# Kernel optimization log

Measured on AMD Instinct MI355X. Metric: run time of the kernel, lower is better.

The kernel has to match this reference:

```python
import jax, jax.numpy as jnp
import numpy as np

B, T, D, H = 4, 1024, 1024, 16


def setup_inputs() -> dict:
    key = jax.random.key(0)
    ks = jax.random.split(key, 6)
    s = 0.02  # small init so softmax is well-conditioned
    return {
        "x": jax.random.normal(ks[0], (B, T, D), jnp.float32),
        "position_embedding": jax.random.normal(ks[1], (B, T, D), jnp.float32),
        "Wc": jax.random.normal(ks[2], (2 * D, D), jnp.float32) * s,
        "bc": jnp.zeros((2 * D,), jnp.float32),
        "Wp": jax.random.normal(ks[3], (D, D), jnp.float32) * s,
        "bp": jnp.zeros((D,), jnp.float32),
        "Wo": jax.random.normal(ks[4], (D, D), jnp.float32) * s,
        "bo": jnp.zeros((D,), jnp.float32),
        "num_heads": H,
    }


def reference(x, position_embedding, Wc, bc, Wp, bp, Wo, bo, num_heads):
    b, t, d = x.shape
    h = num_heads
    hd = d // h
    scale = hd ** -0.5
    # content projection -> q, k  (value reuses content k, as in the original)
    cqk = (x @ Wc.T + bc).reshape(b, t, 2, h, hd)
    q = cqk[:, :, 0]  # [B,T,H,hd]
    k = cqk[:, :, 1]  # [B,T,H,hd]
    # position keys
    pk = (position_embedding @ Wp.T + bp).reshape(b, t, h, hd)
    # dual-stream scores: content-content + content-position
    scores = (jnp.einsum('bqhd,bkhd->bhqk', q, k)
              + jnp.einsum('bqhd,bkhd->bhqk', q, pk)) * scale
    attn = jax.nn.softmax(scores, axis=-1)  # dropout is identity in eval
    out = jnp.einsum('bhqk,bkhd->bqhd', attn, k).reshape(b, t, d)
    return out @ Wo.T + bo, attn
```

## Files before the change

### kernel.cpp

```cpp
#include <hip/hip_runtime.h>
#include <hip/hip_bf16.h>

#define BB 4
#define TT 1024
#define DD 1024
#define HH 16
#define HDIM 64
#define MM (BB*TT)

typedef unsigned short u16;
typedef __attribute__((ext_vector_type(8))) short bf16x8;
typedef __attribute__((ext_vector_type(8))) _Float16 f16x8;
typedef __attribute__((ext_vector_type(4))) float f32x4;
typedef __attribute__((ext_vector_type(4))) unsigned short u16x4;

__device__ __forceinline__ u16 f2bf(float f) {
    union { float f; unsigned u; } v; v.f = f;
    return (u16)((v.u + 0x7fffu + ((v.u >> 16) & 1u)) >> 16);
}
__device__ __forceinline__ float bf2f(u16 h) {
    union { unsigned u; float f; } v; v.u = ((unsigned)h) << 16; return v.f;
}
__device__ __forceinline__ u16 f2h(float f) {
    union { _Float16 h; u16 u; } v; v.h = (_Float16)f;
    return v.u;
}

__device__ __forceinline__ void gload16(const void* g, void* l) {
    __builtin_amdgcn_global_load_lds(
        (const __attribute__((address_space(1))) unsigned int*)g,
        (__attribute__((address_space(3))) unsigned int*)l, 16, 0, 0);
}

__device__ __forceinline__ void cvt_body(const float* __restrict__ src,
                                         u16* __restrict__ dst,
                                         int bid, bool to_fp16)
{
    const size_t i = ((size_t)bid * 256 + threadIdx.x) * 4;
    const float4 v = *(const float4*)&src[i];
    u16x4 o;
    if (to_fp16) { o[0] = f2h(v.x); o[1] = f2h(v.y); o[2] = f2h(v.z); o[3] = f2h(v.w); }
    else         { o[0] = f2bf(v.x); o[1] = f2bf(v.y); o[2] = f2bf(v.z); o[3] = f2bf(v.w); }
    *(u16x4*)&dst[i] = o;
}

__global__ __launch_bounds__(256)
void cvt1_kernel(const float* __restrict__ x, u16* __restrict__ x16,
                 const float* __restrict__ Wc, u16* __restrict__ Wc16)
{
    const int bid = blockIdx.x;
    if (bid < 4096) cvt_body(x, x16, bid, true);
    else            cvt_body(Wc, Wc16, bid - 4096, true);
}

__global__ __launch_bounds__(256)
void cvt2_kernel(const float* __restrict__ pe, u16* __restrict__ pe16,
                 const float* __restrict__ Wp, u16* __restrict__ Wp16,
                 const float* __restrict__ Wo, u16* __restrict__ Wo16)
{
    const int bid = blockIdx.x;
    if (bid < 4096)      cvt_body(pe, pe16, bid, true);
    else if (bid < 5120) cvt_body(Wp, Wp16, bid - 4096, true);
    else                 cvt_body(Wo, Wo16, bid - 5120, false);
}

__global__ __launch_bounds__(256)
void ktrans_kernel(const u16* __restrict__ k16, u16* __restrict__ k16T)
{
    __shared__ u16 tmp[64][72];
    const int tc = blockIdx.x, h = blockIdx.y, b = blockIdx.z;
    const size_t hb = ((size_t)(b * HH + h)) << 16;
    const int tid = threadIdx.x;
    const int sr = tid >> 2, sc = (tid & 3) * 8;
    *(bf16x8*)&tmp[sr][sc]      = *(const bf16x8*)&k16[hb + (size_t)(tc * 64 + sr) * HDIM + sc];
    *(bf16x8*)&tmp[sr][sc + 32] = *(const bf16x8*)&k16[hb + (size_t)(tc * 64 + sr) * HDIM + sc + 32];
    __syncthreads();
#pragma unroll
    for (int half = 0; half < 2; ++half) {
        bf16x8 v;
#pragma unroll
        for (int j = 0; j < 8; ++j) v[j] = (short)tmp[sc + half * 32 + j][sr];
        *(bf16x8*)&k16T[hb + (size_t)sr * TT + tc * 64 + sc + half * 32] = v;
    }
}

template<bool FP16, int MODE>
__global__ __launch_bounds__(256)
void gemm_mfma(const u16* __restrict__ Ah, const u16* __restrict__ Bh,
               const float* __restrict__ bias,
               float* __restrict__ dstF, u16* __restrict__ dstH1,
               const u16* __restrict__ kaux16,
               const int M, const int N, const int K)
{
    __shared__ u16 As[128][64];
    __shared__ u16 Bs[128][64];

    const int tid  = threadIdx.x;
    const int w    = tid >> 6;
    const int lane = tid & 63;
    const int lg   = lane >> 4;
    const int lr   = lane & 15;
    const int wr   = w >> 1, wc = w & 1;
    const int m0   = blockIdx.y * 128, n0 = blockIdx.x * 128;

    const f32x4 zero = {0.f, 0.f, 0.f, 0.f};
    f32x4 acc[4][4];
#pragma unroll
    for (int i = 0; i < 4; ++i)
#pragma unroll
        for (int j = 0; j < 4; ++j) acc[i][j] = zero;

    const int srow = tid >> 3;
    const int scol = (tid & 7) * 8;
    const int ldr  = w << 3;

    for (int k0 = 0; k0 < K; k0 += 64) {
        __syncthreads();
#pragma unroll
        for (int i = 0; i < 4; ++i) {
            const size_t ga = (size_t)(m0 + i * 32 + srow) * K + k0 + scol;
            const size_t gb = (size_t)(n0 + i * 32 + srow) * K + k0 + scol;
            gload16(&Ah[ga], &As[i * 32 + ldr][0]);
            gload16(&Bh[gb], &Bs[i * 32 + ldr][0]);
        }
        __syncthreads();
#pragma unroll
        for (int kk = 0; kk < 2; ++kk) {
            const int koff = kk * 32 + lg * 8;
#pragma unroll
            for (int mf = 0; mf < 4; ++mf) {
#pragma unroll
                for (int nf = 0; nf < 4; ++nf) {
                    if constexpr (FP16) {
                        const f16x8 a = *(const f16x8*)&As[wr * 64 + mf * 16 + lr][koff];
                        const f16x8 b = *(const f16x8*)&Bs[wc * 64 + nf * 16 + lr][koff];
                        acc[mf][nf] = __builtin_amdgcn_mfma_f32_16x16x32_f16(a, b, acc[mf][nf], 0, 0, 0);
                    } else {
                        const bf16x8 a = *(const bf16x8*)&As[wr * 64 + mf * 16 + lr][koff];
                        const bf16x8 b = *(const bf16x8*)&Bs[wc * 64 + nf * 16 + lr][koff];
                        acc[mf][nf] = __builtin_amdgcn_mfma_f32_16x16x32_bf16(a, b, acc[mf][nf], 0, 0, 0);
                    }
                }
            }
        }
    }

#pragma unroll
    for (int mf = 0; mf < 4; ++mf)
#pragma unroll
        for (int nf = 0; nf < 4; ++nf)
#pragma unroll
            for (int j = 0; j < 4; ++j) {
                const int gm = m0 + wr * 64 + mf * 16 + lg * 4 + j;
                const int gn = n0 + wc * 64 + nf * 16 + lr;
                const float v = acc[mf][nf][j] + bias[gn];
                if constexpr (MODE == 0) {
                    const int bb = gm >> 10, t = gm & 1023;
                    const int c = gn >> 10, hh = (gn & 1023) >> 6, d = gn & 63;
                    const size_t idx = ((((size_t)bb * HH + hh) << 10) + t) * HDIM + d;
                    if (c == 0) dstH1[idx] = f2bf(v * 0.125f);
                    else        ((u16*)dstF)[idx] = f2bf(v);
                } else if constexpr (MODE == 1) {
                    const int bb = gm >> 10, t = gm & 1023;
                    const int hh = gn >> 6, d = gn & 63;
                    const size_t idx = ((((size_t)bb * HH + hh) << 10) + t) * HDIM + d;
                    dstH1[idx] = f2bf(v + bf2f(kaux16[idx]));
                } else {
                    dstF[(size_t)gm * N + gn] = v;
                }
            }
}

__global__ __launch_bounds__(256)
void attn_mfma(const u16* __restrict__ qg, const u16* __restrict__ kTg,
               const u16* __restrict__ kpg,
               float* __restrict__ attn, u16* __restrict__ ch)
{
    __shared__ u16 kp_s[2][64][72];
    __shared__ u16 kT_s[2][64][72];
    __shared__ u16 P_s[4][16][72];

    const int tid  = threadIdx.x;
    const int w    = tid >> 6;
    const int lane = tid & 63;
    const int lg   = lane >> 4;
    const int lr   = lane & 15;

    const int fid = blockIdx.x;
    const int c   = fid & 7;
    const int s   = fid >> 3;
    const int g   = c + 8 * (s >> 4);
    const int q0  = (s & 15) * 64;
    const int b   = g >> 4, h = g & 15;
    const size_t hb = ((size_t)(b * HH + h)) << 16;

    bf16x8 qf0, qf1;
    {
        const size_t base = hb + (size_t)(q0 + w * 16 + lr) * HDIM + lg * 8;
        qf0 = *(const bf16x8*)&qg[base];
        qf1 = *(const bf16x8*)&qg[base + 32];
    }

    const int sr = tid >> 2;
    const int sc = (tid & 3) * 8;
    bf16x8 ra, rb, rc, rd;

    ra = *(const bf16x8*)&kpg[hb + (size_t)sr * HDIM + sc];
    rb = *(const bf16x8*)&kpg[hb + (size_t)sr * HDIM + sc + 32];
    *(bf16x8*)&kp_s[0][sr][sc]      = ra;
    *(bf16x8*)&kp_s[0][sr][sc + 32] = rb;
    __syncthreads();

    float rs[4] = {0.f, 0.f, 0.f, 0.f};
    for (int t = 0; t < TT / 64; ++t) {
        const int cur = t & 1;
        if (t < 15) {
            const size_t nb = hb + (size_t)((t + 1) * 64 + sr) * HDIM;
            ra = *(const bf16x8*)&kpg[nb + sc];
            rb = *(const bf16x8*)&kpg[nb + sc + 32];
        }
#pragma unroll
        for (int ct = 0; ct < 4; ++ct) {
            f32x4 acc = {0.f, 0.f, 0.f, 0.f};
            const bf16x8 b0 = *(const bf16x8*)&kp_s[cur][ct * 16 + lr][lg * 8];
            const bf16x8 b1 = *(const bf16x8*)&kp_s[cur][ct * 16 + lr][lg * 8 + 32];
            acc = __builtin_amdgcn_mfma_f32_16x16x32_bf16(qf0, b0, acc, 0, 0, 0);
            acc = __builtin_amdgcn_mfma_f32_16x16x32_bf16(qf1, b1, acc, 0, 0, 0);
#pragma unroll
            for (int j = 0; j < 4; ++j) rs[j] += __expf(acc[j]);
        }
        if (t < 15) {
            *(bf16x8*)&kp_s[cur ^ 1][sr][sc]      = ra;
            *(bf16x8*)&kp_s[cur ^ 1][sr][sc + 32] = rb;
        }
        __syncthreads();
    }

    ra = *(const bf16x8*)&kpg[hb + (size_t)sr * HDIM + sc];
    rb = *(const bf16x8*)&kpg[hb + (size_t)sr * HDIM + sc + 32];
    rc = *(const bf16x8*)&kTg[hb + (size_t)sr * TT + sc];
    rd = *(const bf16x8*)&kTg[hb + (size_t)sr * TT + sc + 32];
#pragma unroll
    for (int off = 1; off < 16; off <<= 1) {
#pragma unroll
        for (int j = 0; j < 4; ++j) rs[j] += __shfl_xor(rs[j], off);
    }
    float ri[4];
#pragma unroll
    for (int j = 0; j < 4; ++j) ri[j] = 1.f / rs[j];
    *(bf16x8*)&kp_s[0][sr][sc]      = ra;
    *(bf16x8*)&kp_s[0][sr][sc + 32] = rb;
    *(bf16x8*)&kT_s[0][sr][sc]      = rc;
    *(bf16x8*)&kT_s[0][sr][sc + 32] = rd;
    __syncthreads();

    f32x4 cacc[4] = {{0,0,0,0},{0,0,0,0},{0,0,0,0},{0,0,0,0}};
    const size_t abase = ((((size_t)b * HH + h) << 10) + q0 + w * 16) << 10;

    for (int t = 0; t < TT / 64; ++t) {
        const int cur = t & 1;
        if (t < 15) {
            const size_t nb = hb + (size_t)((t + 1) * 64 + sr) * HDIM;
            ra = *(const bf16x8*)&kpg[nb + sc];
            rb = *(const bf16x8*)&kpg[nb + sc + 32];
            const size_t tb = hb + (size_t)sr * TT + (t + 1) * 64;
            rc = *(const bf16x8*)&kTg[tb + sc];
            rd = *(const bf16x8*)&kTg[tb + sc + 32];
        }
#pragma unroll
        for (int ct = 0; ct < 4; ++ct) {
            f32x4 acc = {0.f, 0.f, 0.f, 0.f};
            const bf16x8 b0 = *(const bf16x8*)&kp_s[cur][ct * 16 + lr][lg * 8];
            const bf16x8 b1 = *(const bf16x8*)&kp_s[cur][ct * 16 + lr][lg * 8 + 32];
            acc = __builtin_amdgcn_mfma_f32_16x16x32_bf16(qf0, b0, acc, 0, 0, 0);
            acc = __builtin_amdgcn_mfma_f32_16x16x32_bf16(qf1, b1, acc, 0, 0, 0);
            const int col = t * 64 + ct * 16 + lr;
#pragma unroll
            for (int j = 0; j < 4; ++j) {
                const float p = __expf(acc[j]) * ri[j];
                __builtin_nontemporal_store(p, &attn[abase + (size_t)(lg * 4 + j) * TT + col]);
                P_s[w][lg * 4 + j][ct * 16 + lr] = f2bf(p);
            }
        }
        asm volatile("s_waitcnt lgkmcnt(0)" ::: "memory");
        const bf16x8 pa0 = *(const bf16x8*)&P_s[w][lr][lg * 8];
        const bf16x8 pa1 = *(const bf16x8*)&P_s[w][lr][lg * 8 + 32];
#pragma unroll
        for (int dt = 0; dt < 4; ++dt) {
            const bf16x8 kb0 = *(const bf16x8*)&kT_s[cur][dt * 16 + lr][lg * 8];
            const bf16x8 kb1 = *(const bf16x8*)&kT_s[cur][dt * 16 + lr][lg * 8 + 32];
            cacc[dt] = __builtin_amdgcn_mfma_f32_16x16x32_bf16(pa0, kb0, cacc[dt], 0, 0, 0);
            cacc[dt] = __builtin_amdgcn_mfma_f32_16x16x32_bf16(pa1, kb1, cacc[dt], 0, 0, 0);
        }
        if (t < 15) {
            *(bf16x8*)&kp_s[cur ^ 1][sr][sc]      = ra;
            *(bf16x8*)&kp_s[cur ^ 1][sr][sc + 32] = rb;
            *(bf16x8*)&kT_s[cur ^ 1][sr][sc]      = rc;
            *(bf16x8*)&kT_s[cur ^ 1][sr][sc + 32] = rd;
        }
        __syncthreads();
    }

#pragma unroll
    for (int dt = 0; dt < 4; ++dt)
#pragma unroll
        for (int j = 0; j < 4; ++j) {
            const int qr = q0 + w * 16 + lg * 4 + j;
            ch[(((size_t)b << 10) + qr) * DD + h * HDIM + dt * 16 + lr] = f2bf(cacc[dt][j]);
        }
}

extern "C" void kernel_launch(void* const* d_in, const int* in_sizes, int n_in,
                              void* d_out, int out_size, void* d_ws, size_t ws_size,
                              hipStream_t stream)
{
    const float* x  = (const float*)d_in[0];
    const float* pe = (const float*)d_in[1];
    const float* Wc = (const float*)d_in[2];
    const float* bc = (const float*)d_in[3];
    const float* Wp = (const float*)d_in[4];
    const float* bp = (const float*)d_in[5];
    const float* Wo = (const float*)d_in[6];
    const float* bo = (const float*)d_in[7];

    float* out  = (float*)d_out;
    float* attn = out + (size_t)MM * DD;

    char* ws = (char*)d_ws;
    u16* Wp16 = (u16*)(ws);
    u16* q16  = (u16*)(ws + ((size_t)16 << 20));
    u16* k16  = (u16*)(ws + ((size_t)24 << 20));
    u16* kp16 = (u16*)(ws + ((size_t)32 << 20));
    u16* x16  = (u16*)(ws + ((size_t)40 << 20));
    u16* Wo16 = (u16*)(ws + ((size_t)48 << 20));
    u16* Wc16 = (u16*)(ws + ((size_t)56 << 20));
    u16* k16T = (u16*)(ws + ((size_t)56 << 20));
    u16* pe16 = x16;
    u16* chh  = x16;

    cvt1_kernel<<<6144, 256, 0, stream>>>(x, x16, Wc, Wc16);
    gemm_mfma<true, 0><<<dim3(16, 32), 256, 0, stream>>>(
        x16, Wc16, bc, (float*)k16, q16, nullptr, MM, 2048, DD);
    ktrans_kernel<<<dim3(16, HH, BB), 256, 0, stream>>>(k16, k16T);
    cvt2_kernel<<<6144, 256, 0, stream>>>(pe, pe16, Wp, Wp16, Wo, Wo16);
    gemm_mfma<true, 1><<<dim3(8, 32), 256, 0, stream>>>(
        pe16, Wp16, bp, nullptr, kp16, k16, MM, 1024, DD);
    attn_mfma<<<1024, 256, 0, stream>>>(q16, k16T, kp16, attn, chh);
    gemm_mfma<false, 2><<<dim3(8, 32), 256, 0, stream>>>(
        chh, Wo16, bo, out, nullptr, nullptr, MM, 1024, DD);
}
```

Before: 195.8 us.

## Merge conversion kernels and double attention query tile to 8 waves

Result: slower. 220.6 us (+12.7%).

```diff
diff --git a/kernel.cpp b/kernel.cpp
--- a/kernel.cpp
+++ b/kernel.cpp
@@ -45,23 +45,18 @@
 }
 
 __global__ __launch_bounds__(256)
-void cvt1_kernel(const float* __restrict__ x, u16* __restrict__ x16,
-                 const float* __restrict__ Wc, u16* __restrict__ Wc16)
+void cvt_all_kernel(const float* __restrict__ x,  u16* __restrict__ x16,
+                    const float* __restrict__ pe, u16* __restrict__ pe16,
+                    const float* __restrict__ Wc, u16* __restrict__ Wc16,
+                    const float* __restrict__ Wp, u16* __restrict__ Wp16,
+                    const float* __restrict__ Wo, u16* __restrict__ Wo16)
 {
     const int bid = blockIdx.x;
-    if (bid < 4096) cvt_body(x, x16, bid, true);
-    else            cvt_body(Wc, Wc16, bid - 4096, true);
-}
-
-__global__ __launch_bounds__(256)
-void cvt2_kernel(const float* __restrict__ pe, u16* __restrict__ pe16,
-                 const float* __restrict__ Wp, u16* __restrict__ Wp16,
-                 const float* __restrict__ Wo, u16* __restrict__ Wo16)
-{
-    const int bid = blockIdx.x;
-    if (bid < 4096)      cvt_body(pe, pe16, bid, true);
-    else if (bid < 5120) cvt_body(Wp, Wp16, bid - 4096, true);
-    else                 cvt_body(Wo, Wo16, bid - 5120, false);
+    if (bid < 4096)       cvt_body(x,  x16,  bid,        true);
+    else if (bid < 8192)  cvt_body(pe, pe16, bid - 4096, true);
+    else if (bid < 10240) cvt_body(Wc, Wc16, bid - 8192, true);
+    else if (bid < 11264) cvt_body(Wp, Wp16, bid - 10240, true);
+    else                  cvt_body(Wo, Wo16, bid - 11264, false);
 }
 
 __global__ __launch_bounds__(256)
@@ -171,14 +166,14 @@
             }
 }
 
-__global__ __launch_bounds__(256)
+__global__ __launch_bounds__(512)
 void attn_mfma(const u16* __restrict__ qg, const u16* __restrict__ kTg,
                const u16* __restrict__ kpg,
                float* __restrict__ attn, u16* __restrict__ ch)
 {
     __shared__ u16 kp_s[2][64][72];
     __shared__ u16 kT_s[2][64][72];
-    __shared__ u16 P_s[4][16][72];
+    __shared__ u16 P_s[8][16][72];
 
     const int tid  = threadIdx.x;
     const int w    = tid >> 6;
@@ -189,8 +184,8 @@
     const int fid = blockIdx.x;
     const int c   = fid & 7;
     const int s   = fid >> 3;
-    const int g   = c + 8 * (s >> 4);
-    const int q0  = (s & 15) * 64;
+    const int g   = c + 8 * (s >> 3);
+    const int q0  = (s & 7) * 128;
     const int b   = g >> 4, h = g & 15;
     const size_t hb = ((size_t)(b * HH + h)) << 16;
 
@@ -201,23 +196,19 @@
         qf1 = *(const bf16x8*)&qg[base + 32];
     }
 
-    const int sr = tid >> 2;
-    const int sc = (tid & 3) * 8;
-    bf16x8 ra, rb, rc, rd;
+    const int sr = tid >> 3;
+    const int sc = (tid & 7) * 8;
+    bf16x8 ra, rc;
 
     ra = *(const bf16x8*)&kpg[hb + (size_t)sr * HDIM + sc];
-    rb = *(const bf16x8*)&kpg[hb + (size_t)sr * HDIM + sc + 32];
-    *(bf16x8*)&kp_s[0][sr][sc]      = ra;
-    *(bf16x8*)&kp_s[0][sr][sc + 32] = rb;
+    *(bf16x8*)&kp_s[0][sr][sc] = ra;
     __syncthreads();
 
     float rs[4] = {0.f, 0.f, 0.f, 0.f};
     for (int t = 0; t < TT / 64; ++t) {
         const int cur = t & 1;
         if (t < 15) {
-            const size_t nb = hb + (size_t)((t + 1) * 64 + sr) * HDIM;
-            ra = *(const bf16x8*)&kpg[nb + sc];
-            rb = *(const bf16x8*)&kpg[nb + sc + 32];
+            ra = *(const bf16x8*)&kpg[hb + (size_t)((t + 1) * 64 + sr) * HDIM + sc];
         }
 #pragma unroll
         for (int ct = 0; ct < 4; ++ct) {
@@ -230,16 +221,13 @@
             for (int j = 0; j < 4; ++j) rs[j] += __expf(acc[j]);
         }
         if (t < 15) {
-            *(bf16x8*)&kp_s[cur ^ 1][sr][sc]      = ra;
-            *(bf16x8*)&kp_s[cur ^ 1][sr][sc + 32] = rb;
+            *(bf16x8*)&kp_s[cur ^ 1][sr][sc] = ra;
         }
         __syncthreads();
     }
 
     ra = *(const bf16x8*)&kpg[hb + (size_t)sr * HDIM + sc];
-    rb = *(const bf16x8*)&kpg[hb + (size_t)sr * HDIM + sc + 32];
     rc = *(const bf16x8*)&kTg[hb + (size_t)sr * TT + sc];
-    rd = *(const bf16x8*)&kTg[hb + (size_t)sr * TT + sc + 32];
 #pragma unroll
     for (int off = 1; off < 16; off <<= 1) {
 #pragma unroll
@@ -248,10 +236,8 @@
     float ri[4];
 #pragma unroll
     for (int j = 0; j < 4; ++j) ri[j] = 1.f / rs[j];
-    *(bf16x8*)&kp_s[0][sr][sc]      = ra;
-    *(bf16x8*)&kp_s[0][sr][sc + 32] = rb;
-    *(bf16x8*)&kT_s[0][sr][sc]      = rc;
-    *(bf16x8*)&kT_s[0][sr][sc + 32] = rd;
+    *(bf16x8*)&kp_s[0][sr][sc] = ra;
+    *(bf16x8*)&kT_s[0][sr][sc] = rc;
     __syncthreads();
 
     f32x4 cacc[4] = {{0,0,0,0},{0,0,0,0},{0,0,0,0},{0,0,0,0}};
@@ -260,12 +246,8 @@
     for (int t = 0; t < TT / 64; ++t) {
         const int cur = t & 1;
         if (t < 15) {
-            const size_t nb = hb + (size_t)((t + 1) * 64 + sr) * HDIM;
-            ra = *(const bf16x8*)&kpg[nb + sc];
-            rb = *(const bf16x8*)&kpg[nb + sc + 32];
-            const size_t tb = hb + (size_t)sr * TT + (t + 1) * 64;
-            rc = *(const bf16x8*)&kTg[tb + sc];
-            rd = *(const bf16x8*)&kTg[tb + sc + 32];
+            ra = *(const bf16x8*)&kpg[hb + (size_t)((t + 1) * 64 + sr) * HDIM + sc];
+            rc = *(const bf16x8*)&kTg[hb + (size_t)sr * TT + (t + 1) * 64 + sc];
         }
 #pragma unroll
         for (int ct = 0; ct < 4; ++ct) {
@@ -293,10 +275,8 @@
             cacc[dt] = __builtin_amdgcn_mfma_f32_16x16x32_bf16(pa1, kb1, cacc[dt], 0, 0, 0);
         }
         if (t < 15) {
-            *(bf16x8*)&kp_s[cur ^ 1][sr][sc]      = ra;
-            *(bf16x8*)&kp_s[cur ^ 1][sr][sc + 32] = rb;
-            *(bf16x8*)&kT_s[cur ^ 1][sr][sc]      = rc;
-            *(bf16x8*)&kT_s[cur ^ 1][sr][sc + 32] = rd;
+            *(bf16x8*)&kp_s[cur ^ 1][sr][sc] = ra;
+            *(bf16x8*)&kT_s[cur ^ 1][sr][sc] = rc;
         }
         __syncthreads();
     }
@@ -327,25 +307,25 @@
     float* attn = out + (size_t)MM * DD;
 
     char* ws = (char*)d_ws;
-    u16* Wp16 = (u16*)(ws);
-    u16* q16  = (u16*)(ws + ((size_t)16 << 20));
-    u16* k16  = (u16*)(ws + ((size_t)24 << 20));
-    u16* kp16 = (u16*)(ws + ((size_t)32 << 20));
-    u16* x16  = (u16*)(ws + ((size_t)40 << 20));
-    u16* Wo16 = (u16*)(ws + ((size_t)48 << 20));
-    u16* Wc16 = (u16*)(ws + ((size_t)56 << 20));
+    u16* x16  = (u16*)(ws);
+    u16* pe16 = (u16*)(ws + ((size_t)8 << 20));
+    u16* Wc16 = (u16*)(ws + ((size_t)16 << 20));
+    u16* Wp16 = (u16*)(ws + ((size_t)20 << 20));
+    u16* Wo16 = (u16*)(ws + ((size_t)22 << 20));
+    u16* q16  = (u16*)(ws + ((size_t)24 << 20));
+    u16* k16  = (u16*)(ws + ((size_t)32 << 20));
+    u16* kp16 = (u16*)(ws + ((size_t)40 << 20));
     u16* k16T = (u16*)(ws + ((size_t)56 << 20));
-    u16* pe16 = x16;
     u16* chh  = x16;
 
-    cvt1_kernel<<<6144, 256, 0, stream>>>(x, x16, Wc, Wc16);
+    cvt_all_kernel<<<12288, 256, 0, stream>>>(x, x16, pe, pe16, Wc, Wc16,
+                                              Wp, Wp16, Wo, Wo16);
     gemm_mfma<true, 0><<<dim3(16, 32), 256, 0, stream>>>(
         x16, Wc16, bc, (float*)k16, q16, nullptr, MM, 2048, DD);
     ktrans_kernel<<<dim3(16, HH, BB), 256, 0, stream>>>(k16, k16T);
-    cvt2_kernel<<<6144, 256, 0, stream>>>(pe, pe16, Wp, Wp16, Wo, Wo16);
     gemm_mfma<true, 1><<<dim3(8, 32), 256, 0, stream>>>(
         pe16, Wp16, bp, nullptr, kp16, k16, MM, 1024, DD);
-    attn_mfma<<<1024, 256, 0, stream>>>(q16, k16T, kp16, attn, chh);
+    attn_mfma<<<512, 512, 0, stream>>>(q16, k16T, kp16, attn, chh);
     gemm_mfma<false, 2><<<dim3(8, 32), 256, 0, stream>>>(
         chh, Wo16, bo, out, nullptr, nullptr, MM, 1024, DD);
 }
```
